# Optimization experiments

Hardware: AMD Instinct MI355X
Metric: run time of the kernel (lower is better)

## Reference

```python
import jax, jax.numpy as jnp
import numpy as np
from jax.experimental.jet import jet

ORDER = 3  # Taylor order from init_kwargs
D, C, H = 4096, 4096, 8192


def setup_inputs() -> dict:
    key = jax.random.key(0)
    k = jax.random.split(key, 6)
    sc1 = 1.0 / np.sqrt(D + C)
    sc2 = 1.0 / np.sqrt(H)
    return {
        "h": jax.random.normal(k[0], (D,), jnp.float32),
        "r": jnp.zeros((), jnp.float32),  # ignored residual slot of h_r tuple
        "t": jax.random.uniform(k[1], (), jnp.float32),
        "c": jax.random.normal(k[2], (C,), jnp.float32),
        "W1": jax.random.normal(k[3], (D + C, H), jnp.float32) * sc1,
        "b1": jnp.zeros((H,), jnp.float32),
        "W2": jax.random.normal(k[4], (H, D), jnp.float32) * sc2,
        "b2": jnp.zeros((D,), jnp.float32),
    }


def reference(h, r, t, c, W1, b1, W2, b2):
    # dynamics f(h, t, c): 2-layer tanh MLP on concat(h, c)
    def f(_h, _t, _c):
        x = jnp.concatenate((_h, _c))
        return jnp.tanh(x @ W1 + b1) @ W2 + b2

    h_shape = h.shape

    def g(h_t):
        # expand flattened state+time through dynamics
        _h, _t = jnp.reshape(h_t[:-1], h_shape), h_t[-1]
        dh = jnp.ravel(f(_h, _t, c))
        return jnp.concatenate((dh, jnp.array([1.0], dtype=dh.dtype)))

    h_t = jnp.concatenate((jnp.ravel(h), jnp.reshape(t, (1,))))
    # recursive Taylor-mode jet expansion
    (y0, [*yns]) = jet(g, (h_t,), ((jnp.ones_like(h_t),),))
    for _ in range(ORDER - 1):
        (y0, [*yns]) = jet(g, (h_t,), ((y0, *yns),))
    dydt = jnp.reshape(y0[:-1], h_shape)
    drdt = jnp.reshape(yns[-2][:-1], h_shape)
    return (dydt, jnp.mean(drdt ** 2))
```

## Files before the change

kernel.cpp:

```cpp
#include <hip/hip_runtime.h>

#define DD 4096
#define HH 8192

enum Stage { S_X0 = 0, S_TANH, S_BIASOUT, S_PMUL, S_COPY, S_S2 };

template <int STAGE, int KS, int SPREV, int KPREV, int NTOT, int BX>
__global__ __launch_bounds__(256) void gemv_phase(
    const float* __restrict__ W, const float* __restrict__ Pprev,
    float* __restrict__ Pout,
    const float* __restrict__ h, const float* __restrict__ c,
    const float* __restrict__ b1, const float* __restrict__ b2,
    float* __restrict__ s0g, float* __restrict__ t0g, float* __restrict__ a1g,
    float* __restrict__ outv)
{
    constexpr int GROUPS = 256 / KS;
    __shared__ float xs[KS];
    __shared__ float part[GROUPS * KS];
    const int tid = threadIdx.x;
    const int bx = blockIdx.x;
    const int by = blockIdx.y;
    const int k0 = by * KS;

    if constexpr (STAGE == S_X0) {
        if (tid < KS) {
            int k = k0 + tid;
            xs[tid] = (k < DD) ? h[k] : c[k - DD];
        }
    } else {
        const int g = tid / KS, j = tid % KS;
        float acc = 0.f;
        for (int s = g; s < SPREV; s += GROUPS)
            acc += Pprev[(size_t)s * KPREV + k0 + j];
        part[g * KS + j] = acc;
        __syncthreads();
        if (tid < KS) {
            const int k = k0 + tid;
            float tot = 0.f;
#pragma unroll
            for (int g2 = 0; g2 < GROUPS; ++g2) tot += part[g2 * KS + tid];
            float xv;
            if constexpr (STAGE == S_TANH) {
                float s = tanhf(tot + b1[k]);
                xv = s;
                if (bx == 0) { s0g[k] = s; t0g[k] = 1.f - s * s; }
            } else if constexpr (STAGE == S_BIASOUT) {
                xv = tot + b2[k];
                if (bx == 0) outv[k] = xv;
            } else if constexpr (STAGE == S_PMUL) {
                xv = t0g[k] * tot;
                if (bx == 0) a1g[k] = tot;
            } else if constexpr (STAGE == S_COPY) {
                xv = tot;
            } else {
                float a1v = a1g[k];
                xv = t0g[k] * (tot - s0g[k] * a1v * a1v);
            }
            xs[tid] = xv;
        }
    }
    __syncthreads();

    const int ncol = bx * 2048 + tid * 4;
    const float* Wp = W + (size_t)k0 * NTOT + ncol;
    float a0 = 0.f, a1 = 0.f, a2 = 0.f, a3 = 0.f;
    float b0 = 0.f, b1r = 0.f, b2r = 0.f, b3 = 0.f;
#pragma unroll 4
    for (int k = 0; k < KS; ++k) {
        const float xv = xs[k];
        const float* row = Wp + (size_t)k * NTOT;
        const float4 w0 = *reinterpret_cast<const float4*>(row);
        const float4 w1 = *reinterpret_cast<const float4*>(row + 1024);
        a0 = fmaf(xv, w0.x, a0);
        a1 = fmaf(xv, w0.y, a1);
        a2 = fmaf(xv, w0.z, a2);
        a3 = fmaf(xv, w0.w, a3);
        b0 = fmaf(xv, w1.x, b0);
        b1r = fmaf(xv, w1.y, b1r);
        b2r = fmaf(xv, w1.z, b2r);
        b3 = fmaf(xv, w1.w, b3);
    }
    float* op = Pout + (size_t)by * NTOT + ncol;
    *reinterpret_cast<float4*>(op)        = make_float4(a0, a1, a2, a3);
    *reinterpret_cast<float4*>(op + 1024) = make_float4(b0, b1r, b2r, b3);
}

template <int SPREV>
__global__ __launch_bounds__(256) void reduce_sq_partial(const float* __restrict__ P6,
                                                         float* __restrict__ partial) {
    const int n = blockIdx.x * 256 + threadIdx.x;
    float acc = 0.f;
#pragma unroll 8
    for (int s = 0; s < SPREV; ++s) acc += P6[(size_t)s * DD + n];
    float sq = acc * acc;
    for (int off = 32; off; off >>= 1) sq += __shfl_down(sq, off);
    __shared__ float ls[4];
    const int wid = threadIdx.x >> 6;
    if ((threadIdx.x & 63) == 0) ls[wid] = sq;
    __syncthreads();
    if (threadIdx.x == 0) partial[blockIdx.x] = ls[0] + ls[1] + ls[2] + ls[3];
}

__global__ __launch_bounds__(64) void finalize_meansq(const float* __restrict__ partial,
                                                      float* __restrict__ dout) {
    float v = (threadIdx.x < 16) ? partial[threadIdx.x] : 0.f;
    for (int off = 8; off; off >>= 1) v += __shfl_down(v, off);
    if (threadIdx.x == 0) dout[DD] = v / (float)DD;
}

extern "C" void kernel_launch(void* const* d_in, const int* in_sizes, int n_in,
                              void* d_out, int out_size, void* d_ws, size_t ws_size,
                              hipStream_t stream) {
    const float* h  = (const float*)d_in[0];
    const float* c  = (const float*)d_in[3];
    const float* W1 = (const float*)d_in[4];
    const float* b1 = (const float*)d_in[5];
    const float* W2 = (const float*)d_in[6];
    const float* b2 = (const float*)d_in[7];
    float* out = (float*)d_out;
    float* ws = (float*)d_ws;

    float* P1 = ws;
    float* P2 = P1 + 2097152;
    float* P3 = P2 + 2097152;
    float* P4 = P3 + 2097152;
    float* P5 = P4 + 2097152;
    float* P6 = P5 + 2097152;
    float* s0 = P6 + 2097152;
    float* t0 = s0 + 8192;
    float* a1 = t0 + 8192;
    float* psum = a1 + 8192;

    gemv_phase<S_X0, 32, 1, 1, HH, 4><<<dim3(4, 256), 256, 0, stream>>>(
        W1, nullptr, P1, h, c, b1, b2, s0, t0, a1, out);
    gemv_phase<S_TANH, 16, 256, HH, DD, 2><<<dim3(2, 512), 256, 0, stream>>>(
        W2, P1, P2, h, c, b1, b2, s0, t0, a1, out);
    gemv_phase<S_BIASOUT, 16, 512, DD, HH, 4><<<dim3(4, 256), 256, 0, stream>>>(
        W1, P2, P3, h, c, b1, b2, s0, t0, a1, out);
    gemv_phase<S_PMUL, 16, 256, HH, DD, 2><<<dim3(2, 512), 256, 0, stream>>>(
        W2, P3, P4, h, c, b1, b2, s0, t0, a1, out);
    gemv_phase<S_COPY, 16, 512, DD, HH, 4><<<dim3(4, 256), 256, 0, stream>>>(
        W1, P4, P5, h, c, b1, b2, s0, t0, a1, out);
    gemv_phase<S_S2, 16, 256, HH, DD, 2><<<dim3(2, 512), 256, 0, stream>>>(
        W2, P5, P6, h, c, b1, b2, s0, t0, a1, out);
    reduce_sq_partial<512><<<16, 256, 0, stream>>>(P6, psum);
    finalize_meansq<<<1, 64, 0, stream>>>(psum, out);
}
```

Before: 226.2 us.

## Use nontemporal weight loads selectively and retile GEMV phases for fewer partials

Each thread now handles one float4 column group instead of two, K-slices are doubled, and grids are reshaped, which halves the partial-sum buffers and the cross-block reduction work. Weight loads can use nontemporal hints, chosen per phase: the last pass over each matrix, and the half of W1 that is read only once, bypass caching so the reused weights stay resident in the large last-level cache. The cost is less per-thread work and ILP in the inner loop and more per-phase tuning complexity.

```diff
diff --git a/kernel.cpp b/kernel.cpp
--- a/kernel.cpp
+++ b/kernel.cpp
@@ -5,7 +5,31 @@
 
 enum Stage { S_X0 = 0, S_TANH, S_BIASOUT, S_PMUL, S_COPY, S_S2 };
 
-template <int STAGE, int KS, int SPREV, int KPREV, int NTOT, int BX>
+typedef float vfloat4 __attribute__((ext_vector_type(4)));
+
+template <bool NT, int KS, int NTOT>
+__device__ inline void stream_cols(const float* __restrict__ Wp,
+                                   const float* __restrict__ xs,
+                                   float* __restrict__ op) {
+    float ax = 0.f, ay = 0.f, az = 0.f, aw = 0.f;
+#pragma unroll 8
+    for (int k = 0; k < KS; ++k) {
+        const float xv = xs[k];
+        const float* row = Wp + (size_t)k * NTOT;
+        vfloat4 w;
+        if constexpr (NT)
+            w = __builtin_nontemporal_load(reinterpret_cast<const vfloat4*>(row));
+        else
+            w = *reinterpret_cast<const vfloat4*>(row);
+        ax = fmaf(xv, w.x, ax);
+        ay = fmaf(xv, w.y, ay);
+        az = fmaf(xv, w.z, az);
+        aw = fmaf(xv, w.w, aw);
+    }
+    *reinterpret_cast<float4*>(op) = make_float4(ax, ay, az, aw);
+}
+
+template <int STAGE, int KS, int SPREV, int KPREV, int NTOT, int BX, int NTMODE>
 __global__ __launch_bounds__(256) void gemv_phase(
     const float* __restrict__ W, const float* __restrict__ Pprev,
     float* __restrict__ Pout,
@@ -61,28 +85,18 @@
     }
     __syncthreads();
 
-    const int ncol = bx * 2048 + tid * 4;
+    const int ncol = bx * 1024 + tid * 4;
     const float* Wp = W + (size_t)k0 * NTOT + ncol;
-    float a0 = 0.f, a1 = 0.f, a2 = 0.f, a3 = 0.f;
-    float b0 = 0.f, b1r = 0.f, b2r = 0.f, b3 = 0.f;
-#pragma unroll 4
-    for (int k = 0; k < KS; ++k) {
-        const float xv = xs[k];
-        const float* row = Wp + (size_t)k * NTOT;
-        const float4 w0 = *reinterpret_cast<const float4*>(row);
-        const float4 w1 = *reinterpret_cast<const float4*>(row + 1024);
-        a0 = fmaf(xv, w0.x, a0);
-        a1 = fmaf(xv, w0.y, a1);
-        a2 = fmaf(xv, w0.z, a2);
-        a3 = fmaf(xv, w0.w, a3);
-        b0 = fmaf(xv, w1.x, b0);
-        b1r = fmaf(xv, w1.y, b1r);
-        b2r = fmaf(xv, w1.z, b2r);
-        b3 = fmaf(xv, w1.w, b3);
+    float* op = Pout + (size_t)by * NTOT + ncol;
+
+    if constexpr (NTMODE == 0) {
+        stream_cols<false, KS, NTOT>(Wp, xs, op);
+    } else if constexpr (NTMODE == 1) {
+        stream_cols<true, KS, NTOT>(Wp, xs, op);
+    } else {
+        if (k0 >= DD) stream_cols<true, KS, NTOT>(Wp, xs, op);
+        else          stream_cols<false, KS, NTOT>(Wp, xs, op);
     }
-    float* op = Pout + (size_t)by * NTOT + ncol;
-    *reinterpret_cast<float4*>(op)        = make_float4(a0, a1, a2, a3);
-    *reinterpret_cast<float4*>(op + 1024) = make_float4(b0, b1r, b2r, b3);
 }
 
 template <int SPREV>
@@ -121,28 +135,28 @@
     float* ws = (float*)d_ws;
 
     float* P1 = ws;
-    float* P2 = P1 + 2097152;
-    float* P3 = P2 + 2097152;
-    float* P4 = P3 + 2097152;
-    float* P5 = P4 + 2097152;
-    float* P6 = P5 + 2097152;
-    float* s0 = P6 + 2097152;
+    float* P2 = P1 + 1048576;
+    float* P3 = P2 + 1048576;
+    float* P4 = P3 + 1048576;
+    float* P5 = P4 + 1048576;
+    float* P6 = P5 + 1048576;
+    float* s0 = P6 + 1048576;
     float* t0 = s0 + 8192;
     float* a1 = t0 + 8192;
     float* psum = a1 + 8192;
 
-    gemv_phase<S_X0, 32, 1, 1, HH, 4><<<dim3(4, 256), 256, 0, stream>>>(
+    gemv_phase<S_X0, 64, 1, 1, HH, 8, 2><<<dim3(8, 128), 256, 0, stream>>>(
         W1, nullptr, P1, h, c, b1, b2, s0, t0, a1, out);
-    gemv_phase<S_TANH, 16, 256, HH, DD, 2><<<dim3(2, 512), 256, 0, stream>>>(
+    gemv_phase<S_TANH, 32, 128, HH, DD, 4, 0><<<dim3(4, 256), 256, 0, stream>>>(
         W2, P1, P2, h, c, b1, b2, s0, t0, a1, out);
-    gemv_phase<S_BIASOUT, 16, 512, DD, HH, 4><<<dim3(4, 256), 256, 0, stream>>>(
+    gemv_phase<S_BIASOUT, 32, 256, DD, HH, 8, 0><<<dim3(8, 128), 256, 0, stream>>>(
         W1, P2, P3, h, c, b1, b2, s0, t0, a1, out);
-    gemv_phase<S_PMUL, 16, 256, HH, DD, 2><<<dim3(2, 512), 256, 0, stream>>>(
+    gemv_phase<S_PMUL, 32, 128, HH, DD, 4, 0><<<dim3(4, 256), 256, 0, stream>>>(
         W2, P3, P4, h, c, b1, b2, s0, t0, a1, out);
-    gemv_phase<S_COPY, 16, 512, DD, HH, 4><<<dim3(4, 256), 256, 0, stream>>>(
+    gemv_phase<S_COPY, 32, 256, DD, HH, 8, 1><<<dim3(8, 128), 256, 0, stream>>>(
         W1, P4, P5, h, c, b1, b2, s0, t0, a1, out);
-    gemv_phase<S_S2, 16, 256, HH, DD, 2><<<dim3(2, 512), 256, 0, stream>>>(
+    gemv_phase<S_S2, 32, 128, HH, DD, 4, 1><<<dim3(4, 256), 256, 0, stream>>>(
         W2, P5, P6, h, c, b1, b2, s0, t0, a1, out);
-    reduce_sq_partial<512><<<16, 256, 0, stream>>>(P6, psum);
+    reduce_sq_partial<256><<<16, 256, 0, stream>>>(P6, psum);
     finalize_meansq<<<1, 64, 0, stream>>>(psum, out);
 }
```

Measured after the change: 212.0 us. 6.3% less time.
